# Optimization experiments

Measured on AMD Instinct MI355X. Metric: run time of the kernel, lower is better.

The kernel has to match this reference:

```python
import jax, jax.numpy as jnp
import numpy as np

C = 64
CK = C // 8  # query/key channels

def setup_inputs() -> dict:
    key = jax.random.key(0)
    ks = jax.random.split(key, 8)
    x = jax.random.normal(ks[0], (4, C, 16, 16, 16), dtype=jnp.float32)
    # 1x1x1 Conv3d weights collapse to [out_ch, in_ch] matrices
    wq = jax.random.normal(ks[1], (CK, C), dtype=jnp.float32) * (1.0 / np.sqrt(C))
    bq = jax.random.normal(ks[2], (CK,), dtype=jnp.float32) * 0.01
    wk = jax.random.normal(ks[3], (CK, C), dtype=jnp.float32) * (1.0 / np.sqrt(C))
    bk = jax.random.normal(ks[4], (CK,), dtype=jnp.float32) * 0.01
    wv = jax.random.normal(ks[5], (C, C), dtype=jnp.float32) * (1.0 / np.sqrt(C))
    bv = jax.random.normal(ks[6], (C,), dtype=jnp.float32) * 0.01
    gamma = jnp.ones((1,), dtype=jnp.float32) * 0.5  # nonzero so attention path affects output
    return {"x": x, "wq": wq, "bq": bq, "wk": wk, "bk": bk, "wv": wv, "bv": bv, "gamma": gamma}

def reference(x, wq, bq, wk, bk, wv, bv, gamma):
    B, Cc, D, H, W = x.shape
    N = D * H * W
    xf = x.reshape(B, Cc, N)  # [B, C, N]
    q = jnp.einsum('kc,bcn->bkn', wq, xf) + bq[None, :, None]  # [B, CK, N]
    k = jnp.einsum('kc,bcn->bkn', wk, xf) + bk[None, :, None]  # [B, CK, N]
    v = jnp.einsum('oc,bcn->bon', wv, xf) + bv[None, :, None]  # [B, C, N]
    # energy[b,i,j] = sum_k q[b,k,i] * k[b,k,j]; softmax over j (no scaling, per source)
    energy = jnp.einsum('bki,bkj->bij', q, k)  # [B, N, N]
    attn = jax.nn.softmax(energy, axis=-1)
    # out[b,c,i] = sum_j v[b,c,j] * attn[b,i,j]
    out = jnp.einsum('bcj,bij->bci', v, attn)  # [B, C, N]
    out = out.reshape(B, Cc, D, H, W)
    return gamma * out + x
```

## Files before the change

### kernel.cpp

```cpp
#include <hip/hip_runtime.h>
#include <hip/hip_bf16.h>

#define BATCH  4
#define CDIM   64
#define CKD    8
#define NPOS   4096
#define RLN2   1.44269504f
#define SH2    25.96851039f
#define ECL2   14.42695041f
#define PTP    72

typedef _Float16 f16x8 __attribute__((ext_vector_type(8)));
typedef float    f32x4 __attribute__((ext_vector_type(4)));

__device__ __forceinline__ f16x8 pack8(const float* e) {
    f16x8 v;
#pragma unroll
    for (int i = 0; i < 8; ++i) v[i] = (_Float16)e[i];
    return v;
}

__global__ __launch_bounds__(256, 4) void proj_kernel(
    const float* __restrict__ x,
    const float* __restrict__ wq, const float* __restrict__ bq,
    const float* __restrict__ wk, const float* __restrict__ bk,
    const float* __restrict__ wv, const float* __restrict__ bv,
    _Float16* __restrict__ qh, _Float16* __restrict__ kh,
    _Float16* __restrict__ vswz)
{
    __shared__ float red[64 * 73];

    const int bid  = blockIdx.x;
    const int part = bid >> 8;
    const int tid  = threadIdx.x;
    const int s    = tid & 63;
    const int h    = tid >> 6;
    const int pos  = (bid & 255) * 64 + s;
    const int b    = pos >> 12;
    const int n    = pos & 4095;
    const int c0   = part * 16;
    const int cl0  = h * 16;

    const float* xb = x + (size_t)b * CDIM * NPOS + n;

    float vacc[16];
#pragma unroll
    for (int o = 0; o < 16; ++o) vacc[o] = 0.f;
    float qacc[8] = {0.f, 0.f, 0.f, 0.f, 0.f, 0.f, 0.f, 0.f};

    if (part < 2) {
        const float* wqk = (part == 0) ? wq : wk;
#pragma unroll
        for (int cc = 0; cc < 16; ++cc) {
            const int c = cl0 + cc;
            const float xv = xb[(size_t)c * NPOS];
#pragma unroll
            for (int o = 0; o < 8; ++o)  qacc[o] = fmaf(wqk[o * CDIM + c], xv, qacc[o]);
#pragma unroll
            for (int o = 0; o < 16; ++o) vacc[o] = fmaf(wv[(c0 + o) * CDIM + c], xv, vacc[o]);
        }
    } else {
#pragma unroll
        for (int cc = 0; cc < 16; ++cc) {
            const int c = cl0 + cc;
            const float xv = xb[(size_t)c * NPOS];
#pragma unroll
            for (int o = 0; o < 16; ++o) vacc[o] = fmaf(wv[(c0 + o) * CDIM + c], xv, vacc[o]);
        }
    }

    float* rs = red + s * 73;
    if (h != 0) {
        float* rh = rs + (h - 1) * 24;
        if (part < 2) {
#pragma unroll
            for (int i = 0; i < 8; ++i)  rh[i] = qacc[i];
#pragma unroll
            for (int o = 0; o < 16; ++o) rh[8 + o] = vacc[o];
        } else {
#pragma unroll
            for (int o = 0; o < 16; ++o) rh[o] = vacc[o];
        }
    }
    __syncthreads();
    if (h != 0) return;

    if (part < 2) {
#pragma unroll
        for (int i = 0; i < 8; ++i)  qacc[i] += rs[i] + rs[24 + i] + rs[48 + i];
#pragma unroll
        for (int o = 0; o < 16; ++o) vacc[o] += rs[8 + o] + rs[32 + o] + rs[56 + o];

        const float* bqk = (part == 0) ? bq : bk;
        const float scl  = (part == 0) ? RLN2 : 1.0f;
        f16x8 qv;
#pragma unroll
        for (int o = 0; o < 8; ++o) qv[o] = (_Float16)((qacc[o] + bqk[o]) * scl);
        _Float16* dst = ((part == 0) ? qh : kh) + ((size_t)(b * NPOS + n)) * CKD;
        *(f16x8*)dst = qv;
    } else {
#pragma unroll
        for (int o = 0; o < 16; ++o) vacc[o] += rs[o] + rs[24 + o] + rs[48 + o];
    }

    const int jq = (n >> 2) & 3;
    const int ju = ((n >> 4) & 1) * 4 + (n & 3);
    const size_t vbase = (size_t)(b * 128 + (n >> 5)) * 2048 + jq * 8 + ju;
#pragma unroll
    for (int o = 0; o < 16; ++o)
        vswz[vbase + (size_t)(c0 + o) * 32] = (_Float16)(vacc[o] + bv[c0 + o]);
}

template<int NSPLIT>
__global__ __launch_bounds__(256, 4) void attn_kernel(
    const _Float16* __restrict__ qh, const _Float16* __restrict__ kh,
    const _Float16* __restrict__ vswz,
    __hip_bfloat16* __restrict__ po, float* __restrict__ pl)
{
    constexpr int JCHUNK = NPOS / NSPLIT;
    constexpr int NIT32  = JCHUNK / 32;

    __shared__ __hip_bfloat16 pt[4][16][PTP];

    const int bid   = blockIdx.x;
    const int split = bid & (NSPLIT - 1);
    const int itile = (bid / NSPLIT) & 31;
    const int b     = bid / (NSPLIT * 32);
    const int tid   = threadIdx.x;
    const int wave  = tid >> 6;
    const int lane  = tid & 63;
    const int quad  = lane >> 4;
    const int m16   = lane & 15;

    const int i0 = itile * 128 + wave * 32;

    f16x8 qa0 = *(const f16x8*)(qh + ((size_t)(b * NPOS + i0 + m16)) * CKD);
    f16x8 qa1 = *(const f16x8*)(qh + ((size_t)(b * NPOS + i0 + 16 + m16)) * CKD);
    if (quad != 0) { qa0 = (f16x8){}; qa1 = (f16x8){}; }

    const _Float16* kp = kh + ((size_t)(b * NPOS + split * JCHUNK) + (size_t)m16) * CKD;
    const _Float16* vp = vswz + (size_t)b * 262144
                       + (size_t)split * (JCHUNK / 32) * 2048
                       + (size_t)(m16 * 32 + quad * 8);

    f32x4 acc0[4], acc1[4];
#pragma unroll
    for (int nb = 0; nb < 4; ++nb) {
        acc0[nb] = (f32x4){0.f, 0.f, 0.f, 0.f};
        acc1[nb] = (f32x4){0.f, 0.f, 0.f, 0.f};
    }
    float ls0 = 0.f, ls1 = 0.f;
    const f32x4 csh = {-SH2, -SH2, -SH2, -SH2};

#pragma unroll 2
    for (int it = 0; it < NIT32; ++it) {
        const f16x8 kfa = *(const f16x8*)kp;
        const f16x8 kfb = *(const f16x8*)(kp + 16 * CKD);

        const f32x4 s0a = __builtin_amdgcn_mfma_f32_16x16x32_f16(kfa, qa0, csh, 0, 0, 0);
        const f32x4 s0b = __builtin_amdgcn_mfma_f32_16x16x32_f16(kfb, qa0, csh, 0, 0, 0);
        const f32x4 s1a = __builtin_amdgcn_mfma_f32_16x16x32_f16(kfa, qa1, csh, 0, 0, 0);
        const f32x4 s1b = __builtin_amdgcn_mfma_f32_16x16x32_f16(kfb, qa1, csh, 0, 0, 0);

        float e0[8], e1[8];
#pragma unroll
        for (int r = 0; r < 4; ++r) {
            e0[r]     = __builtin_exp2f(fminf(s0a[r], ECL2));
            e0[4 + r] = __builtin_exp2f(fminf(s0b[r], ECL2));
            e1[r]     = __builtin_exp2f(fminf(s1a[r], ECL2));
            e1[4 + r] = __builtin_exp2f(fminf(s1b[r], ECL2));
        }
        ls0 += ((e0[0] + e0[1]) + (e0[2] + e0[3])) + ((e0[4] + e0[5]) + (e0[6] + e0[7]));
        ls1 += ((e1[0] + e1[1]) + (e1[2] + e1[3])) + ((e1[4] + e1[5]) + (e1[6] + e1[7]));

        const f16x8 pa0 = pack8(e0);
        const f16x8 pa1 = pack8(e1);

#pragma unroll
        for (int nb = 0; nb < 4; ++nb) {
            const f16x8 vb = *(const f16x8*)(vp + (size_t)nb * 512);
            acc0[nb] = __builtin_amdgcn_mfma_f32_16x16x32_f16(pa0, vb, acc0[nb], 0, 0, 0);
            acc1[nb] = __builtin_amdgcn_mfma_f32_16x16x32_f16(pa1, vb, acc1[nb], 0, 0, 0);
        }
        kp += 32 * CKD;
        vp += 2048;
    }

    ls0 += __shfl_xor(ls0, 16);
    ls0 += __shfl_xor(ls0, 32);
    ls1 += __shfl_xor(ls1, 16);
    ls1 += __shfl_xor(ls1, 32);

    const int sbx = split * BATCH + b;
    if (quad == 0) {
        pl[(size_t)sbx * NPOS + i0 + m16]      = ls0;
        pl[(size_t)sbx * NPOS + i0 + 16 + m16] = ls1;
    }

    __hip_bfloat16* ept = &pt[wave][0][0];

#define EPILOG(ACC, IOFS)                                                     \
    do {                                                                      \
        _Pragma("unroll")                                                     \
        for (int nb = 0; nb < 4; ++nb)                                        \
            _Pragma("unroll")                                                 \
            for (int r = 0; r < 4; ++r)                                       \
                ept[(quad * 4 + r) * PTP + nb * 16 + m16] =                   \
                    __float2bfloat16(ACC[nb][r]);                             \
        _Pragma("unroll")                                                     \
        for (int g2 = 0; g2 < 16; ++g2) {                                     \
            const int c = quad + g2 * 4;                                      \
            po[((size_t)sbx * CDIM + c) * NPOS + i0 + (IOFS) + m16] =         \
                ept[m16 * PTP + c];                                           \
        }                                                                     \
    } while (0)

    EPILOG(acc0, 0);
    EPILOG(acc1, 16);
#undef EPILOG
}

template<int NSPLIT>
__global__ __launch_bounds__(256) void combine_kernel(
    const float* __restrict__ x,
    const __hip_bfloat16* __restrict__ po, const float* __restrict__ pl,
    const float* __restrict__ gamma, float* __restrict__ out)
{
    const int t  = blockIdx.x * 256 + threadIdx.x;
    const int i4 = (t & 1023) * 4;
    const int c  = (t >> 10) & 63;
    const int b  = t >> 16;

    const unsigned short* pou = (const unsigned short*)po;

    float L0 = 0.f, L1 = 0.f, L2 = 0.f, L3 = 0.f;
    float O0 = 0.f, O1 = 0.f, O2 = 0.f, O3 = 0.f;
#pragma unroll
    for (int s = 0; s < NSPLIT; ++s) {
        const size_t sb = (size_t)(s * BATCH + b);
        const float4 lv = *(const float4*)(pl + sb * NPOS + i4);
        const ushort4 pv = *(const ushort4*)(pou + (sb * CDIM + c) * NPOS + i4);
        L0 += lv.x; L1 += lv.y; L2 += lv.z; L3 += lv.w;
        O0 += __uint_as_float((unsigned)pv.x << 16);
        O1 += __uint_as_float((unsigned)pv.y << 16);
        O2 += __uint_as_float((unsigned)pv.z << 16);
        O3 += __uint_as_float((unsigned)pv.w << 16);
    }
    const float g = gamma[0];
    const size_t xi = ((size_t)(b * CDIM + c)) * NPOS + i4;
    const float4 xv = *(const float4*)(x + xi);
    float4 o;
    o.x = fmaf(g, O0 / L0, xv.x);
    o.y = fmaf(g, O1 / L1, xv.y);
    o.z = fmaf(g, O2 / L2, xv.z);
    o.w = fmaf(g, O3 / L3, xv.w);
    *(float4*)(out + xi) = o;
}

extern "C" void kernel_launch(void* const* d_in, const int* in_sizes, int n_in,
                              void* d_out, int out_size, void* d_ws, size_t ws_size,
                              hipStream_t stream)
{
    const float* x     = (const float*)d_in[0];
    const float* wq    = (const float*)d_in[1];
    const float* bq    = (const float*)d_in[2];
    const float* wk    = (const float*)d_in[3];
    const float* bk    = (const float*)d_in[4];
    const float* wv    = (const float*)d_in[5];
    const float* bv    = (const float*)d_in[6];
    const float* gamma = (const float*)d_in[7];
    float* out = (float*)d_out;

    char* ws = (char*)d_ws;
    _Float16*       qh   = (_Float16*)(ws);
    _Float16*       kh   = (_Float16*)(ws + (256 << 10));
    _Float16*       vswz = (_Float16*)(ws + (512 << 10));
    __hip_bfloat16* po   = (__hip_bfloat16*)(ws + (2560 << 10));

    const size_t po8_end = (2560ull << 10) + 8ull * 4 * CDIM * NPOS * 2;
    const size_t need8   = po8_end + 8ull * 4 * NPOS * 4;

    proj_kernel<<<1024, 256, 0, stream>>>(x, wq, bq, wk, bk, wv, bv, qh, kh, vswz);

    if (ws_size >= need8) {
        float* pl = (float*)(ws + po8_end);
        attn_kernel<8><<<BATCH * 32 * 8, 256, 0, stream>>>(qh, kh, vswz, po, pl);
        combine_kernel<8><<<4096 / 4, 256, 0, stream>>>(x, po, pl, gamma, out);
    } else {
        const size_t po4_end = (2560ull << 10) + 4ull * 4 * CDIM * NPOS * 2;
        float* pl = (float*)(ws + po4_end);
        attn_kernel<4><<<BATCH * 32 * 4, 256, 0, stream>>>(qh, kh, vswz, po, pl);
        combine_kernel<4><<<4096 / 4, 256, 0, stream>>>(x, po, pl, gamma, out);
    }
}
```

Measured before the change: 124.1 us.

## Stage K and V tiles through double-buffered LDS with direct global-to-LDS loads

```diff
diff --git a/kernel.cpp b/kernel.cpp
--- a/kernel.cpp
+++ b/kernel.cpp
@@ -18,6 +18,17 @@
 #pragma unroll
     for (int i = 0; i < 8; ++i) v[i] = (_Float16)e[i];
     return v;
+}
+
+__device__ __forceinline__ void gl_lds16(const void* g, void* l) {
+    __builtin_amdgcn_global_load_lds(
+        (const __attribute__((address_space(1))) void*)g,
+        (__attribute__((address_space(3))) void*)l, 16, 0, 0);
+}
+__device__ __forceinline__ void gl_lds4(const void* g, void* l) {
+    __builtin_amdgcn_global_load_lds(
+        (const __attribute__((address_space(1))) void*)g,
+        (__attribute__((address_space(3))) void*)l, 4, 0, 0);
 }
 
 __global__ __launch_bounds__(256, 4) void proj_kernel(
@@ -120,6 +131,8 @@
     constexpr int JCHUNK = NPOS / NSPLIT;
     constexpr int NIT32  = JCHUNK / 32;
 
+    __shared__ __align__(16) _Float16 vbuf[2][2048];
+    __shared__ __align__(16) _Float16 kbuf[2][256];
     __shared__ __hip_bfloat16 pt[4][16][PTP];
 
     const int bid   = blockIdx.x;
@@ -138,10 +151,11 @@
     f16x8 qa1 = *(const f16x8*)(qh + ((size_t)(b * NPOS + i0 + 16 + m16)) * CKD);
     if (quad != 0) { qa0 = (f16x8){}; qa1 = (f16x8){}; }
 
-    const _Float16* kp = kh + ((size_t)(b * NPOS + split * JCHUNK) + (size_t)m16) * CKD;
-    const _Float16* vp = vswz + (size_t)b * 262144
-                       + (size_t)split * (JCHUNK / 32) * 2048
-                       + (size_t)(m16 * 32 + quad * 8);
+    const _Float16* vsrc = vswz + (size_t)b * 262144
+                         + (size_t)split * (JCHUNK / 32) * 2048
+                         + wave * 512 + lane * 8;
+    const _Float16* ksrc = kh + ((size_t)(b * NPOS + split * JCHUNK)) * CKD
+                         + wave * 128 + lane * 2;
 
     f32x4 acc0[4], acc1[4];
 #pragma unroll
@@ -152,15 +166,25 @@
     float ls0 = 0.f, ls1 = 0.f;
     const f32x4 csh = {-SH2, -SH2, -SH2, -SH2};
 
-#pragma unroll 2
+    gl_lds16(vsrc, &vbuf[0][wave * 512]);
+    if (wave < 2) gl_lds4(ksrc, &kbuf[0][wave * 128]);
+    asm volatile("s_waitcnt vmcnt(0)" ::: "memory");
+    __builtin_amdgcn_s_barrier();
+
+    int cur = 0;
     for (int it = 0; it < NIT32; ++it) {
-        const f16x8 kfa = *(const f16x8*)kp;
-        const f16x8 kfb = *(const f16x8*)(kp + 16 * CKD);
-
+        gl_lds16(vsrc + (size_t)(it + 1) * 2048, &vbuf[cur ^ 1][wave * 512]);
+        if (wave < 2) gl_lds4(ksrc + (size_t)(it + 1) * 256, &kbuf[cur ^ 1][wave * 128]);
+
+        const f16x8 kfa = *(const f16x8*)(&kbuf[cur][m16 * 8]);
+        const f16x8 kfb = *(const f16x8*)(&kbuf[cur][128 + m16 * 8]);
+
+        __builtin_amdgcn_s_setprio(1);
         const f32x4 s0a = __builtin_amdgcn_mfma_f32_16x16x32_f16(kfa, qa0, csh, 0, 0, 0);
         const f32x4 s0b = __builtin_amdgcn_mfma_f32_16x16x32_f16(kfb, qa0, csh, 0, 0, 0);
         const f32x4 s1a = __builtin_amdgcn_mfma_f32_16x16x32_f16(kfa, qa1, csh, 0, 0, 0);
         const f32x4 s1b = __builtin_amdgcn_mfma_f32_16x16x32_f16(kfb, qa1, csh, 0, 0, 0);
+        __builtin_amdgcn_s_setprio(0);
 
         float e0[8], e1[8];
 #pragma unroll
@@ -176,14 +200,18 @@
         const f16x8 pa0 = pack8(e0);
         const f16x8 pa1 = pack8(e1);
 
+        __builtin_amdgcn_s_setprio(1);
 #pragma unroll
         for (int nb = 0; nb < 4; ++nb) {
-            const f16x8 vb = *(const f16x8*)(vp + (size_t)nb * 512);
+            const f16x8 vb = *(const f16x8*)(&vbuf[cur][m16 * 32 + quad * 8 + nb * 512]);
             acc0[nb] = __builtin_amdgcn_mfma_f32_16x16x32_f16(pa0, vb, acc0[nb], 0, 0, 0);
             acc1[nb] = __builtin_amdgcn_mfma_f32_16x16x32_f16(pa1, vb, acc1[nb], 0, 0, 0);
         }
-        kp += 32 * CKD;
-        vp += 2048;
+        __builtin_amdgcn_s_setprio(0);
+
+        asm volatile("s_waitcnt vmcnt(0)" ::: "memory");
+        __builtin_amdgcn_s_barrier();
+        cur ^= 1;
     }
 
     ls0 += __shfl_xor(ls0, 16);
@@ -285,11 +313,11 @@
     if (ws_size >= need8) {
         float* pl = (float*)(ws + po8_end);
         attn_kernel<8><<<BATCH * 32 * 8, 256, 0, stream>>>(qh, kh, vswz, po, pl);
-        combine_kernel<8><<<4096 / 4, 256, 0, stream>>>(x, po, pl, gamma, out);
+        combine_kernel<8><<<1024, 256, 0, stream>>>(x, po, pl, gamma, out);
     } else {
         const size_t po4_end = (2560ull << 10) + 4ull * 4 * CDIM * NPOS * 2;
         float* pl = (float*)(ws + po4_end);
         attn_kernel<4><<<BATCH * 32 * 4, 256, 0, stream>>>(qh, kh, vswz, po, pl);
-        combine_kernel<4><<<4096 / 4, 256, 0, stream>>>(x, po, pl, gamma, out);
-    }
-}
+        combine_kernel<4><<<1024, 256, 0, stream>>>(x, po, pl, gamma, out);
+    }
+}
```

Result: no change. 122.2 us (-1.6%).
